# Kernel tuning notes

Hardware: AMD Instinct MI355X
Metric: run time of the kernel (lower is better)

The kernel has to match this reference:

```python
import jax, jax.numpy as jnp
import numpy as np

# Arbitrary non-contiguous kernel tap offsets (constructor arg sk_ind)
SK_IND = np.array([-512, -256, -128, -96, -64, -48, -32, -24, -16, -12, -8, -6,
                   -4, -3, -2, -1, 0, 1, 2, 3, 4, 6, 8, 12, 16, 24, 32, 48,
                   64, 96, 128, 256], dtype=np.int32)
IN_CHANNELS = 64
OUT_CHANNELS = 64
BATCH = 16
INPUT_LEN = 4096


def setup_inputs() -> dict:
    key = jax.random.key(0)
    k1, k2 = jax.random.split(key)
    x = jax.random.normal(k1, (BATCH, IN_CHANNELS, INPUT_LEN), dtype=jnp.float32)
    sk_weights = jax.random.normal(k2, (OUT_CHANNELS, IN_CHANNELS, SK_IND.shape[0]), dtype=jnp.float32)
    return {"x": x, "sk_weights": sk_weights}


def reference(x, sk_weights):
    # x: [B, Cin, L]; sk_weights: [Cout, Cin, K]
    B, C, L = x.shape
    low_pad = max(-int(SK_IND.min()), 0)   # zeros consumed by negative taps
    high_pad = max(int(SK_IND.max()), 0)   # zeros consumed by positive taps
    # Original pads zeros AFTER the signal: [x, zeros(high_pad), zeros(low_pad)];
    # negative numpy indices then wrap into the trailing low_pad zeros.
    padded = jnp.concatenate([x, jnp.zeros((B, C, high_pad + low_pad), x.dtype)], axis=-1)
    padded_len = L + high_pad + low_pad
    idx = SK_IND[:, None] + np.arange(L)                 # [K, L], static
    idx = np.where(idx < 0, padded_len + idx, idx)       # emulate numpy negative-index wrap
    gathered = padded[:, :, idx]                          # [B, Cin, K, L]
    # Per-position GEMM: contract over (Cin, K)
    return jnp.einsum('oik,bikl->bol', sk_weights, gathered)  # [B, Cout, L]
```

## Files before the change

### kernel.cpp

```cpp
#include <hip/hip_runtime.h>


#define B_    16
#define CIN   64
#define COUT  64
#define LEN   4096
#define PAD_LO 512
#define PAD_HI 256
#define LPAD  (LEN + PAD_LO + PAD_HI)
#define NTAP  32

typedef float f32x4 __attribute__((ext_vector_type(4)));
typedef short bf16x8_s __attribute__((ext_vector_type(8)));
typedef __bf16 bf16x8_b __attribute__((ext_vector_type(8)));
typedef unsigned short u16x8 __attribute__((ext_vector_type(8)));

template <typename V>
static __device__ inline auto mfma_16x16x32_bf16(V a, V b, f32x4 c, int)
    -> decltype(__builtin_amdgcn_mfma_f32_16x16x32_bf16(a, b, c, 0, 0, 0)) {
  return __builtin_amdgcn_mfma_f32_16x16x32_bf16(a, b, c, 0, 0, 0);
}
template <typename V>
static __device__ inline f32x4 mfma_16x16x32_bf16(V a, V b, f32x4 c, long) {
  return __builtin_amdgcn_mfma_f32_16x16x32_bf16(
      __builtin_bit_cast(bf16x8_b, a), __builtin_bit_cast(bf16x8_b, b), c, 0, 0, 0);
}

static __device__ inline unsigned short f32_to_bf16_rne(float f) {
  unsigned int u = __builtin_bit_cast(unsigned int, f);
  u += 0x7fffu + ((u >> 16) & 1u);
  return (unsigned short)(u >> 16);
}

static __device__ inline void async_copy16(const void* g, void* l) {
  __builtin_amdgcn_global_load_lds((const __attribute__((address_space(1))) unsigned int*)g,
                                   (__attribute__((address_space(3))) unsigned int*)l, 16, 0, 0);
}

__global__ __launch_bounds__(256) void prep_xw(const float* __restrict__ x,
                                               const float* __restrict__ w,
                                               unsigned short* __restrict__ xp,
                                               unsigned short* __restrict__ wf) {
  __shared__ float tile[64][65];
  const int b = blockIdx.y;
  const int lp0 = blockIdx.x * 64;
  const int tid = threadIdx.x;
  const bool data = (lp0 >= PAD_LO) && (lp0 < PAD_LO + LEN);
  if (data) {
    const int l0 = lp0 - PAD_LO;
#pragma unroll
    for (int it = 0; it < 4; ++it) {
      const int pidx = it * 256 + tid;
      const int il = pidx >> 4;
      const int lq = (pidx & 15) * 4;
      const float4 v = *(const float4*)&x[(size_t)(b * CIN + il) * LEN + l0 + lq];
      tile[lq + 0][il] = v.x;
      tile[lq + 1][il] = v.y;
      tile[lq + 2][il] = v.z;
      tile[lq + 3][il] = v.w;
    }
  } else if (lp0 < PAD_LO) {
    const int base = (b * 8 + blockIdx.x) * 1024;
#pragma unroll
    for (int it = 0; it < 4; ++it) {
      const int e = base + it * 256 + tid;
      const int j = e & 7;
      const int lane = (e >> 3) & 63;
      const int m = (e >> 9) & 3;
      const int c = (e >> 11) & 1;
      const int t = e >> 12;
      const int o = m * 16 + (lane & 15);
      const int i = c * 32 + (lane >> 4) * 8 + j;
      wf[e] = f32_to_bf16_rne(w[(size_t)(o * CIN + i) * NTAP + t]);
    }
  }
  __syncthreads();
#pragma unroll
  for (int it = 0; it < 2; ++it) {
    const int pidx = it * 256 + tid;
    const int ll = pidx >> 3;
    const int i8 = (pidx & 7) * 8;
    u16x8 v = {0, 0, 0, 0, 0, 0, 0, 0};
    if (data) {
#pragma unroll
      for (int j = 0; j < 8; ++j) v[j] = f32_to_bf16_rne(tile[ll][i8 + j]);
    }
    *(u16x8*)&xp[(size_t)(b * LPAD + lp0 + ll) * CIN + i8] = v;
  }
}

__global__ __launch_bounds__(512, 2) void sconv_main(const unsigned short* __restrict__ xp,
                                                     const unsigned short* __restrict__ wf,
                                                     float* __restrict__ out) {
  constexpr int TAP[NTAP] = {-512, -256, -128, -96, -64, -48, -32, -24, -16, -12, -8,
                             -6,   -4,   -3,   -2,  -1,  0,   1,   2,   3,   4,  6,
                             8,    12,   16,   24,  32,  48,  64,  96,  128, 256};
  __shared__ alignas(16) char smem[131072];

  const int id = blockIdx.x;
  const int b = (id & 7) * 2 + (id >> 7);
  const int l0 = ((id >> 3) & 15) * 256;
  const int lb = l0 + PAD_LO;
  const int tid = threadIdx.x;
  const int wv = tid >> 6, lane = tid & 63;
  const int q = lane >> 4, r = lane & 15;
  const int lh = wv >> 1, ch = wv & 1;

  const char* xbase = (const char*)xp + ((size_t)b * LPAD + lb) * (CIN * 2);
  const char* wbase = (const char*)wf;

  auto stageB = [&](int a0, int ng) {
    for (int g = wv; g < ng; g += 8) {
      const int ra = a0 + g * 8 + (lane >> 3);
      const int cs = (lane & 7) ^ (ra & 7);
      const int sb = (lb + a0 + g * 8) & 1023;
      async_copy16(xbase + (ptrdiff_t)ra * 128 + cs * 16, smem + sb * 128);
    }
  };

  bf16x8_s Wreg[2][4], Breg[2][4];
  f32x4 acc[4][4] = {};

  auto loadW = [&](int tt, int p) {
    const char* src = wbase + tt * 8192 + ch * 4096 + lane * 16;
#pragma unroll
    for (int m = 0; m < 4; ++m)
      Wreg[p][m] = *(const bf16x8_s*)(src + m * 1024);
  };
  auto readB = [&](int tt, int p) {
    const int e = (TAP[tt] + r) & 7;
#pragma unroll
    for (int n = 0; n < 4; ++n) {
      const int slot = (lb + TAP[tt] + lh * 64 + 16 * n + r) & 1023;
      Breg[p][n] = *(const bf16x8_s*)(smem + slot * 128 + (((ch * 4 + q) ^ e) << 4));
    }
  };

  loadW(0, 0);
  stageB(-512, 84);

#pragma unroll
  for (int g = 0; g < 8; ++g) {
    __syncthreads();
    readB(4 * g, 0);
    if (g < 7) {
      const int dstart = TAP[4 * g + 3] + 256;
      const int dend = TAP[4 * g + 7] + 256;
      const int a0 = dstart & ~7;
      stageB(a0, (dend - a0 + 7) >> 3);
    }
    __builtin_amdgcn_sched_barrier(0);
#pragma unroll
    for (int u = 0; u < 4; ++u) {
      const int t = 4 * g + u, p = t & 1;
      if (t + 1 < NTAP) {
        loadW(t + 1, p ^ 1);
        if ((t + 1) & 3) readB(t + 1, p ^ 1);
      }
      __builtin_amdgcn_sched_barrier(0);
#pragma unroll
      for (int m = 0; m < 4; ++m)
#pragma unroll
        for (int n = 0; n < 4; ++n)
          acc[m][n] = mfma_16x16x32_bf16(Wreg[p][m], Breg[p][n], acc[m][n], 0);
    }
  }

  __syncthreads();
  if (ch == 1) {
#pragma unroll
    for (int m = 0; m < 4; ++m)
#pragma unroll
      for (int n = 0; n < 4; ++n)
        *(f32x4*)(smem + lh * 16384 + ((m * 4 + n) * 64 + lane) * 16) = acc[m][n];
  }
  __syncthreads();
  if (ch == 0) {
#pragma unroll
    for (int m = 0; m < 4; ++m)
#pragma unroll
      for (int n = 0; n < 4; ++n) {
        const f32x4 other = *(const f32x4*)(smem + lh * 16384 + ((m * 4 + n) * 64 + lane) * 16);
        const f32x4 v = acc[m][n] + other;
#pragma unroll
        for (int d = 0; d < 4; ++d) {
          const int o = 16 * m + 4 * q + d;
          const int l = l0 + lh * 64 + 16 * n + r;
          out[((size_t)b * COUT + o) * LEN + l] = v[d];
        }
      }
  }
}

extern "C" void kernel_launch(void* const* d_in, const int* in_sizes, int n_in,
                              void* d_out, int out_size, void* d_ws, size_t ws_size,
                              hipStream_t stream) {
  const float* x = (const float*)d_in[0];
  const float* w = (const float*)d_in[1];
  float* out = (float*)d_out;

  unsigned short* xp = (unsigned short*)d_ws;
  unsigned short* wfp = xp + (size_t)B_ * LPAD * CIN;

  prep_xw<<<dim3(LPAD / 64, B_), 256, 0, stream>>>(x, w, xp, wfp);
  sconv_main<<<dim3(256), 512, 0, stream>>>(xp, wfp, out);
}
```

Baseline: 89.88 us.

## Shrink output tile to 128 positions, drop channel split, use variable tap chunks

The main conv kernel now handles 128 positions per block with 4 waves instead of 256 positions with 8 waves. Each wave covers both input-channel halves itself, so the cross-wave LDS reduction and its barriers go away. The LDS ring shrinks to 64KB, and staging follows non-uniform tap chunks sized to the tap spacing. Launching 512 smaller blocks is meant to fill more CUs, at the cost of fewer MFMAs per barrier and more redundant weight loads across blocks.

```diff
diff --git a/kernel.cpp b/kernel.cpp
--- a/kernel.cpp
+++ b/kernel.cpp
@@ -89,107 +89,101 @@
   }
 }
 
-__global__ __launch_bounds__(512, 2) void sconv_main(const unsigned short* __restrict__ xp,
+__global__ __launch_bounds__(256, 2) void sconv_main(const unsigned short* __restrict__ xp,
                                                      const unsigned short* __restrict__ wf,
                                                      float* __restrict__ out) {
   constexpr int TAP[NTAP] = {-512, -256, -128, -96, -64, -48, -32, -24, -16, -12, -8,
                              -6,   -4,   -3,   -2,  -1,  0,   1,   2,   3,   4,  6,
                              8,    12,   16,   24,  32,  48,  64,  96,  128, 256};
-  __shared__ alignas(16) char smem[131072];
+  constexpr int NCH = 7;
+  constexpr int CS[NCH + 1] = {0, 1, 2, 4, 8, 16, 24, 32};
+  constexpr int SEND[NCH] = {-385, -129, 31, 103, 126, 135, 383};
+  __shared__ alignas(16) char smem[65536];
 
   const int id = blockIdx.x;
-  const int b = (id & 7) * 2 + (id >> 7);
-  const int l0 = ((id >> 3) & 15) * 256;
+  const int b = (id & 7) * 2 + ((id >> 3) & 1);
+  const int l0 = (id >> 4) * 128;
   const int lb = l0 + PAD_LO;
   const int tid = threadIdx.x;
   const int wv = tid >> 6, lane = tid & 63;
   const int q = lane >> 4, r = lane & 15;
-  const int lh = wv >> 1, ch = wv & 1;
+  const int lh = wv;
 
   const char* xbase = (const char*)xp + ((size_t)b * LPAD + lb) * (CIN * 2);
   const char* wbase = (const char*)wf;
 
   auto stageB = [&](int a0, int ng) {
-    for (int g = wv; g < ng; g += 8) {
+    for (int g = wv; g < ng; g += 4) {
       const int ra = a0 + g * 8 + (lane >> 3);
       const int cs = (lane & 7) ^ (ra & 7);
-      const int sb = (lb + a0 + g * 8) & 1023;
+      const int sb = (lb + a0 + g * 8) & 511;
       async_copy16(xbase + (ptrdiff_t)ra * 128 + cs * 16, smem + sb * 128);
     }
   };
 
-  bf16x8_s Wreg[2][4], Breg[2][4];
-  f32x4 acc[4][4] = {};
+  bf16x8_s Wreg[2][8], Breg[2][4];
+  f32x4 acc[4][2] = {};
 
   auto loadW = [&](int tt, int p) {
-    const char* src = wbase + tt * 8192 + ch * 4096 + lane * 16;
+    const char* src = wbase + tt * 8192 + lane * 16;
 #pragma unroll
     for (int m = 0; m < 4; ++m)
-      Wreg[p][m] = *(const bf16x8_s*)(src + m * 1024);
+#pragma unroll
+      for (int c = 0; c < 2; ++c)
+        Wreg[p][m * 2 + c] = *(const bf16x8_s*)(src + c * 4096 + m * 1024);
   };
   auto readB = [&](int tt, int p) {
     const int e = (TAP[tt] + r) & 7;
 #pragma unroll
-    for (int n = 0; n < 4; ++n) {
-      const int slot = (lb + TAP[tt] + lh * 64 + 16 * n + r) & 1023;
-      Breg[p][n] = *(const bf16x8_s*)(smem + slot * 128 + (((ch * 4 + q) ^ e) << 4));
+    for (int n = 0; n < 2; ++n) {
+      const int slot = (lb + TAP[tt] + lh * 32 + 16 * n + r) & 511;
+#pragma unroll
+      for (int c = 0; c < 2; ++c)
+        Breg[p][n * 2 + c] = *(const bf16x8_s*)(smem + slot * 128 + (((c * 4 + q) ^ e) << 4));
     }
   };
 
   loadW(0, 0);
-  stageB(-512, 84);
-
-#pragma unroll
-  for (int g = 0; g < 8; ++g) {
+  stageB(-512, 16);
+
+#pragma unroll
+  for (int i = 0; i < NCH; ++i) {
     __syncthreads();
-    readB(4 * g, 0);
-    if (g < 7) {
-      const int dstart = TAP[4 * g + 3] + 256;
-      const int dend = TAP[4 * g + 7] + 256;
-      const int a0 = dstart & ~7;
-      stageB(a0, (dend - a0 + 7) >> 3);
+    if (i + 1 < NCH) {
+      const int ds = SEND[i] + 1;
+      const int a0 = ds & ~7;
+      stageB(a0, (SEND[i + 1] + 1 - a0 + 7) >> 3);
     }
     __builtin_amdgcn_sched_barrier(0);
-#pragma unroll
-    for (int u = 0; u < 4; ++u) {
-      const int t = 4 * g + u, p = t & 1;
+    readB(CS[i], CS[i] & 1);
+#pragma unroll
+    for (int t = CS[i]; t < CS[i + 1]; ++t) {
+      const int p = t & 1;
       if (t + 1 < NTAP) {
         loadW(t + 1, p ^ 1);
-        if ((t + 1) & 3) readB(t + 1, p ^ 1);
+        if (t + 1 < CS[i + 1]) readB(t + 1, p ^ 1);
       }
       __builtin_amdgcn_sched_barrier(0);
 #pragma unroll
-      for (int m = 0; m < 4; ++m)
-#pragma unroll
-        for (int n = 0; n < 4; ++n)
-          acc[m][n] = mfma_16x16x32_bf16(Wreg[p][m], Breg[p][n], acc[m][n], 0);
+      for (int c = 0; c < 2; ++c)
+#pragma unroll
+        for (int m = 0; m < 4; ++m)
+#pragma unroll
+          for (int n = 0; n < 2; ++n)
+            acc[m][n] = mfma_16x16x32_bf16(Wreg[p][m * 2 + c], Breg[p][n * 2 + c], acc[m][n], 0);
     }
   }
 
-  __syncthreads();
-  if (ch == 1) {
-#pragma unroll
-    for (int m = 0; m < 4; ++m)
-#pragma unroll
-      for (int n = 0; n < 4; ++n)
-        *(f32x4*)(smem + lh * 16384 + ((m * 4 + n) * 64 + lane) * 16) = acc[m][n];
-  }
-  __syncthreads();
-  if (ch == 0) {
-#pragma unroll
-    for (int m = 0; m < 4; ++m)
-#pragma unroll
-      for (int n = 0; n < 4; ++n) {
-        const f32x4 other = *(const f32x4*)(smem + lh * 16384 + ((m * 4 + n) * 64 + lane) * 16);
-        const f32x4 v = acc[m][n] + other;
-#pragma unroll
-        for (int d = 0; d < 4; ++d) {
-          const int o = 16 * m + 4 * q + d;
-          const int l = l0 + lh * 64 + 16 * n + r;
-          out[((size_t)b * COUT + o) * LEN + l] = v[d];
-        }
+#pragma unroll
+  for (int m = 0; m < 4; ++m)
+#pragma unroll
+    for (int n = 0; n < 2; ++n)
+#pragma unroll
+      for (int d = 0; d < 4; ++d) {
+        const int o = 16 * m + 4 * q + d;
+        const int l = l0 + lh * 32 + 16 * n + r;
+        out[((size_t)b * COUT + o) * LEN + l] = acc[m][n][d];
       }
-  }
 }
 
 extern "C" void kernel_launch(void* const* d_in, const int* in_sizes, int n_in,
@@ -203,5 +197,5 @@
   unsigned short* wfp = xp + (size_t)B_ * LPAD * CIN;
 
   prep_xw<<<dim3(LPAD / 64, B_), 256, 0, stream>>>(x, w, xp, wfp);
-  sconv_main<<<dim3(256), 512, 0, stream>>>(xp, wfp, out);
-}
+  sconv_main<<<dim3(16 * 32), 256, 0, stream>>>(xp, wfp, out);
+}
```

Measured after the change: 92.30 us. 2.7% more time.
